# Kernel tuning notes

Measured on AMD Instinct MI355X. Metric: run time of the kernel, lower is better.

Reference implementation:

```python
import jax, jax.numpy as jnp
import numpy as np

N, E = 50000, 600000
IN, PE, H, L, K = 112, 16, 128, 64, 4


def setup_inputs() -> dict:
    key = jax.random.key(0)
    ks = jax.random.split(key, 8)
    x = jax.random.normal(ks[0], (N, IN), jnp.float32)
    edge_index = jax.random.randint(ks[1], (2, E), 0, N, dtype=jnp.int64)
    lap_pe = jax.random.normal(ks[2], (N, PE), jnp.float32)
    edge_weight = jax.random.uniform(ks[3], (E,), jnp.float32)
    s = lambda k, shp, fan: jax.random.normal(k, shp, jnp.float32) / np.sqrt(fan).astype(np.float32)
    W1 = s(ks[4], (K, IN + PE, H), IN + PE)
    b1 = jnp.zeros((H,), jnp.float32)
    W2 = s(ks[5], (K, H, H), H)
    b2 = jnp.zeros((H,), jnp.float32)
    Wmu = s(ks[6], (H, L), H)
    bmu = jnp.zeros((L,), jnp.float32)
    Wlv = s(ks[7], (H, L), H)
    blv = jnp.zeros((L,), jnp.float32)
    return dict(x=x, edge_index=edge_index, lap_pe=lap_pe, edge_weight=edge_weight,
                W1=W1, b1=b1, W2=W2, b2=b2, Wmu=Wmu, bmu=bmu, Wlv=Wlv, blv=blv)


def _cheb_conv(h, src, dst, w, W, b):
    """PyG ChebConv with precomputed scaled-Laplacian edge weights w.
    T_0 = h ; T_1 = That h ; T_k = 2 That T_{k-1} - T_{k-2}; out = sum_k T_k W_k + b."""
    n = h.shape[0]
    prop = lambda t: jax.ops.segment_sum(w[:, None] * t[src], dst, num_segments=n)
    Tx0 = h
    out = Tx0 @ W[0]
    Tx1 = prop(Tx0)
    out = out + Tx1 @ W[1]
    for k in range(2, W.shape[0]):
        Tx2 = 2.0 * prop(Tx1) - Tx0
        out = out + Tx2 @ W[k]
        Tx0, Tx1 = Tx1, Tx2
    return out + b


def reference(x, edge_index, lap_pe, edge_weight, W1, b1, W2, b2, Wmu, bmu, Wlv, blv):
    n = x.shape[0]
    src, dst = edge_index[0], edge_index[1]
    # sym-normalized Laplacian, lambda_max=2 -> That = L_sym - I = -D^-1/2 A D^-1/2
    deg = jax.ops.segment_sum(edge_weight, src, num_segments=n)
    dis = jnp.where(deg > 0, jax.lax.rsqrt(jnp.maximum(deg, 1e-12)), 0.0)
    w = -dis[src] * edge_weight * dis[dst]
    h = jnp.concatenate([x, lap_pe], axis=1)  # [N, in+pe]
    h = jax.nn.relu(_cheb_conv(h, src, dst, w, W1, b1))
    h = jax.nn.relu(_cheb_conv(h, src, dst, w, W2, b2))
    mu = h @ Wmu + bmu
    logvar = h @ Wlv + blv
    return (mu, logvar)
```

## Files before the change

kernel.cpp:

```cpp
#include <hip/hip_runtime.h>


typedef __bf16 bf16x8 __attribute__((ext_vector_type(8)));
typedef float f32x4 __attribute__((ext_vector_type(4)));
typedef unsigned int uint32;
typedef unsigned short ushort16;

__device__ inline ushort16 f2bf(float f) {
    uint32 x = __float_as_uint(f);
    uint32 r = x + 0x7fffu + ((x >> 16) & 1u);
    return (ushort16)(r >> 16);
}
__device__ inline float bflo(uint32 v) { return __uint_as_float(v << 16); }
__device__ inline float bfhi(uint32 v) { return __uint_as_float(v & 0xffff0000u); }


__global__ void k_deg_cnt(const int* __restrict__ src, const int* __restrict__ dst,
                          const float* __restrict__ ew, float* __restrict__ deg,
                          int* __restrict__ cnt, int* __restrict__ pos, int E) {
    int e = blockIdx.x * blockDim.x + threadIdx.x;
    if (e >= E) return;
    atomicAdd(&deg[src[e]], ew[e]);
    pos[e] = atomicAdd(&cnt[dst[e]], 1);
}

__global__ void k_scan_blk(const int* __restrict__ cnt, int* __restrict__ row_ptr,
                           int* __restrict__ blk_sums, int N) {
    __shared__ int wsum[4];
    const int tid = threadIdx.x;
    const int base = blockIdx.x * 1024 + tid * 4;
    int4 v = make_int4(0, 0, 0, 0);
    if (base + 3 < N) v = *(const int4*)&cnt[base];
    else {
        if (base + 0 < N) v.x = cnt[base + 0];
        if (base + 1 < N) v.y = cnt[base + 1];
        if (base + 2 < N) v.z = cnt[base + 2];
    }
    const int tsum = v.x + v.y + v.z + v.w;
    const int lane = tid & 63;
    const int wv = tid >> 6;
    int incl = tsum;
    #pragma unroll
    for (int off = 1; off < 64; off <<= 1) {
        int t = __shfl_up(incl, off);
        if (lane >= off) incl += t;
    }
    if (lane == 63) wsum[wv] = incl;
    __syncthreads();
    int woff = 0;
    #pragma unroll
    for (int w = 0; w < 4; ++w) if (w < wv) woff += wsum[w];
    const int excl = woff + incl - tsum;
    if (base + 0 < N) row_ptr[base + 0] = excl;
    if (base + 1 < N) row_ptr[base + 1] = excl + v.x;
    if (base + 2 < N) row_ptr[base + 2] = excl + v.x + v.y;
    if (base + 3 < N) row_ptr[base + 3] = excl + v.x + v.y + v.z;
    if (tid == 255) blk_sums[blockIdx.x] = woff + incl;
}

__global__ void k_scan_top(int* __restrict__ blk_sums, int* __restrict__ row_ptr,
                           int nblk, int N) {
    const int lane = threadIdx.x;
    int v = (lane < nblk) ? blk_sums[lane] : 0;
    int incl = v;
    #pragma unroll
    for (int off = 1; off < 64; off <<= 1) {
        int t = __shfl_up(incl, off);
        if (lane >= off) incl += t;
    }
    if (lane < nblk) blk_sums[lane] = incl - v;
    if (lane == 63) row_ptr[N] = incl;
}

__global__ void k_fix_dis(int* __restrict__ row_ptr, const int* __restrict__ blk_sums,
                          const float* __restrict__ deg, float* __restrict__ dis, int N) {
    int i = blockIdx.x * blockDim.x + threadIdx.x;
    if (i >= N) return;
    row_ptr[i] += blk_sums[i >> 10];
    float d = deg[i];
    dis[i] = d > 0.f ? rsqrtf(fmaxf(d, 1e-12f)) : 0.f;
}

__global__ void k_scatter(const int* __restrict__ src, const int* __restrict__ dst,
                          const float* __restrict__ ew, const float* __restrict__ dis,
                          const int* __restrict__ row_ptr, const int* __restrict__ pos,
                          int2* __restrict__ csr, int E) {
    int e = blockIdx.x * blockDim.x + threadIdx.x;
    if (e >= E) return;
    int s = src[e], d = dst[e];
    float wv = -dis[s] * ew[e] * dis[d];
    csr[row_ptr[d] + pos[e]] = make_int2(s, __float_as_int(wv));
}


__global__ void k_concat_bf16(const float* __restrict__ x, const float* __restrict__ pe,
                              uint32* __restrict__ h, int N) {
    int i4 = (blockIdx.x * blockDim.x + threadIdx.x) * 4;
    if (i4 >= N * 64) return;
    int node = i4 >> 6, p = i4 & 63;
    float4 fa, fb;
    if (p < 56) {
        const float* xp = &x[(size_t)node * 112 + p * 2];
        fa = *(const float4*)xp; fb = *(const float4*)(xp + 4);
    } else {
        const float* pp = &pe[(size_t)node * 16 + (p - 56) * 2];
        fa = *(const float4*)pp; fb = *(const float4*)(pp + 4);
    }
    int4 o;
    o.x = (uint32)f2bf(fa.x) | ((uint32)f2bf(fa.y) << 16);
    o.y = (uint32)f2bf(fa.z) | ((uint32)f2bf(fa.w) << 16);
    o.z = (uint32)f2bf(fb.x) | ((uint32)f2bf(fb.y) << 16);
    o.w = (uint32)f2bf(fb.z) | ((uint32)f2bf(fb.w) << 16);
    *(int4*)&h[i4] = o;
}


__device__ inline float wtrans(const float* __restrict__ W, int kb, size_t o) {
    switch (kb) {
        case 0:  return W[o] - W[o + 32768];
        case 1:  return W[o + 16384] - 3.f * W[o + 49152];
        case 2:  return 2.f * W[o + 32768];
        default: return 4.f * W[o + 49152];
    }
}

__global__ void k_pack_all(const float* __restrict__ W1, const float* __restrict__ W2,
                           const float* __restrict__ Wm, const float* __restrict__ Wl,
                           ushort16* __restrict__ W1p, ushort16* __restrict__ W2p,
                           ushort16* __restrict__ WHp) {
    int t = blockIdx.x * blockDim.x + threadIdx.x;
    uint32 v[8];
    if (t < 16384) {
        const float* W = (t < 8192) ? W1 : W2;
        ushort16* Wp = (t < 8192) ? W1p : W2p;
        int tt = t & 8191;
        int l = tt & 63, c = (tt >> 6) & 7, ks = tt >> 9;
        int kb = ks >> 2;
        int r0 = (ks & 3) * 32 + (l >> 4) * 8;
        int col = c * 16 + (l & 15);
        #pragma unroll
        for (int j = 0; j < 8; ++j)
            v[j] = f2bf(wtrans(W, kb, (size_t)(r0 + j) * 128 + col));
        uint4 o;
        o.x = v[0] | (v[1] << 16); o.y = v[2] | (v[3] << 16);
        o.z = v[4] | (v[5] << 16); o.w = v[6] | (v[7] << 16);
        *(uint4*)(Wp + (size_t)tt * 8) = o;
    } else if (t < 16384 + 2048) {
        int tt = t - 16384;
        int l = tt & 63, c = (tt >> 6) & 7, ks = tt >> 9;
        int k0 = ks * 32 + (l >> 4) * 8;
        int cc = c * 16 + (l & 15);
        const float* Ws = (cc < 64) ? Wm : Wl;
        int col = cc & 63;
        #pragma unroll
        for (int j = 0; j < 8; ++j) v[j] = f2bf(Ws[(size_t)(k0 + j) * 64 + col]);
        uint4 o;
        o.x = v[0] | (v[1] << 16); o.y = v[2] | (v[3] << 16);
        o.z = v[4] | (v[5] << 16); o.w = v[6] | (v[7] << 16);
        *(uint4*)(WHp + (size_t)tt * 8) = o;
    }
}


__global__ void k_prop(const uint32* __restrict__ tin, const int2* __restrict__ csr,
                       const int* __restrict__ row_ptr, uint32* __restrict__ out, int N) {
    int wid = (blockIdx.x * blockDim.x + threadIdx.x) >> 6;
    int lane = threadIdx.x & 63;
    if (wid >= N) return;
    int beg = row_ptr[wid], end = row_ptr[wid + 1];
    const int half = lane >> 5;
    const int fl = lane & 31;
    float a0 = 0.f, a1 = 0.f, a2 = 0.f, a3 = 0.f;
    for (int base = beg; base < end; base += 64) {
        int m = end - base; if (m > 64) m = 64;
        int2 ev = (lane < m) ? csr[base + lane] : make_int2(0, 0);
        for (int j = 0; j < m; j += 8) {
            #pragma unroll
            for (int u = 0; u < 4; ++u) {
                int idx = j + u * 2 + half;
                int s = __shfl(ev.x, idx);
                float w = __uint_as_float(__shfl(ev.y, idx));
                uint2 v = *(const uint2*)&tin[(size_t)s * 64 + fl * 2];
                a0 = fmaf(w, bflo(v.x), a0); a1 = fmaf(w, bfhi(v.x), a1);
                a2 = fmaf(w, bflo(v.y), a2); a3 = fmaf(w, bfhi(v.y), a3);
            }
        }
    }
    a0 += __shfl_xor(a0, 32);
    a1 += __shfl_xor(a1, 32);
    a2 += __shfl_xor(a2, 32);
    a3 += __shfl_xor(a3, 32);
    if (lane < 32) {
        uint2 o;
        o.x = (uint32)f2bf(a0) | ((uint32)f2bf(a1) << 16);
        o.y = (uint32)f2bf(a2) | ((uint32)f2bf(a3) << 16);
        *(uint2*)&out[(size_t)wid * 64 + fl * 2] = o;
    }
}


template<bool RELU>
__launch_bounds__(256)
__global__ void k_mfma_gemm512(const ushort16* __restrict__ t0, const ushort16* __restrict__ t1,
                               const ushort16* __restrict__ t2, const ushort16* __restrict__ t3,
                               const ushort16* __restrict__ Wp, const float* __restrict__ bias,
                               ushort16* __restrict__ C, int N) {
    const int lane = threadIdx.x & 63;
    const int wave = threadIdx.x >> 6;
    const int brow = blockIdx.x * 128 + wave * 32;
    int r0 = brow + (lane & 15);
    int r1 = r0 + 16;
    if (r0 >= N) r0 = N - 1;
    if (r1 >= N) r1 = N - 1;
    const int kg8 = (lane >> 4) * 8;
    f32x4 acc[2][8] = {};
    #pragma unroll
    for (int t = 0; t < 4; ++t) {
        const ushort16* __restrict__ A = (t == 0) ? t0 : (t == 1) ? t1 : (t == 2) ? t2 : t3;
        const ushort16* a0p = A + (size_t)r0 * 128 + kg8;
        const ushort16* a1p = A + (size_t)r1 * 128 + kg8;
        #pragma unroll
        for (int ks2 = 0; ks2 < 4; ++ks2) {
            bf16x8 a0 = *(const bf16x8*)(a0p + ks2 * 32);
            bf16x8 a1 = *(const bf16x8*)(a1p + ks2 * 32);
            const ushort16* bp = Wp + (size_t)((t * 4 + ks2) * 8 * 64 + lane) * 8;
            #pragma unroll
            for (int c = 0; c < 8; ++c) {
                bf16x8 b = *(const bf16x8*)(bp + c * 512);
                acc[0][c] = __builtin_amdgcn_mfma_f32_16x16x32_bf16(a0, b, acc[0][c], 0, 0, 0);
                acc[1][c] = __builtin_amdgcn_mfma_f32_16x16x32_bf16(a1, b, acc[1][c], 0, 0, 0);
            }
        }
    }
    const int col0 = lane & 15;
    const int rj = (lane >> 4) * 4;
    #pragma unroll
    for (int m = 0; m < 2; ++m) {
        #pragma unroll
        for (int c = 0; c < 8; ++c) {
            float bv = bias[c * 16 + col0];
            #pragma unroll
            for (int j = 0; j < 4; ++j) {
                int row = brow + m * 16 + rj + j;
                if (row < N) {
                    float v = acc[m][c][j] + bv;
                    if (RELU) v = fmaxf(v, 0.f);
                    C[(size_t)row * 128 + c * 16 + col0] = f2bf(v);
                }
            }
        }
    }
}


__launch_bounds__(256)
__global__ void k_mfma_head(const ushort16* __restrict__ A, const ushort16* __restrict__ Wp,
                            const float* __restrict__ bm, const float* __restrict__ bl,
                            float* __restrict__ out, int N) {
    const int lane = threadIdx.x & 63;
    const int wave = threadIdx.x >> 6;
    const int brow = blockIdx.x * 128 + wave * 32;
    int r0 = brow + (lane & 15);
    int r1 = r0 + 16;
    if (r0 >= N) r0 = N - 1;
    if (r1 >= N) r1 = N - 1;
    const int kg8 = (lane >> 4) * 8;
    f32x4 acc[2][8] = {};
    const ushort16* a0p = A + (size_t)r0 * 128 + kg8;
    const ushort16* a1p = A + (size_t)r1 * 128 + kg8;
    #pragma unroll
    for (int ks = 0; ks < 4; ++ks) {
        bf16x8 a0 = *(const bf16x8*)(a0p + ks * 32);
        bf16x8 a1 = *(const bf16x8*)(a1p + ks * 32);
        const ushort16* bp = Wp + (size_t)(ks * 8 * 64 + lane) * 8;
        #pragma unroll
        for (int c = 0; c < 8; ++c) {
            bf16x8 b = *(const bf16x8*)(bp + c * 512);
            acc[0][c] = __builtin_amdgcn_mfma_f32_16x16x32_bf16(a0, b, acc[0][c], 0, 0, 0);
            acc[1][c] = __builtin_amdgcn_mfma_f32_16x16x32_bf16(a1, b, acc[1][c], 0, 0, 0);
        }
    }
    const int col0 = lane & 15;
    const int rj = (lane >> 4) * 4;
    #pragma unroll
    for (int m = 0; m < 2; ++m) {
        #pragma unroll
        for (int c = 0; c < 8; ++c) {
            int gcol = (c & 3) * 16 + col0;
            float bv = (c < 4) ? bm[gcol] : bl[gcol];
            size_t hoff = (c < 4) ? 0 : (size_t)N * 64;
            #pragma unroll
            for (int j = 0; j < 4; ++j) {
                int row = brow + m * 16 + rj + j;
                if (row < N)
                    out[hoff + (size_t)row * 64 + gcol] = acc[m][c][j] + bv;
            }
        }
    }
}


extern "C" void kernel_launch(void* const* d_in, const int* in_sizes, int n_in,
                              void* d_out, int out_size, void* d_ws, size_t ws_size,
                              hipStream_t stream) {
    const float* x   = (const float*)d_in[0];
    const int*   ei  = (const int*)d_in[1];
    const float* pe  = (const float*)d_in[2];
    const float* ew  = (const float*)d_in[3];
    const float* W1  = (const float*)d_in[4];
    const float* b1  = (const float*)d_in[5];
    const float* W2  = (const float*)d_in[6];
    const float* b2  = (const float*)d_in[7];
    const float* Wmu = (const float*)d_in[8];
    const float* bmu = (const float*)d_in[9];
    const float* Wlv = (const float*)d_in[10];
    const float* blv = (const float*)d_in[11];

    const int N = in_sizes[0] / 112;
    const int E = in_sizes[1] / 2;
    const int* src = ei;
    const int* dst = ei + E;

    char* ws = (char*)d_ws;
    size_t off = 0;
    auto alloc = [&](size_t bytes) -> char* {
        char* p = ws + off;
        off = (off + bytes + 255) & ~(size_t)255;
        return p;
    };
    float* deg     = (float*)alloc((size_t)N * 4);
    int*   cnt     = (int*)  alloc((size_t)N * 4);
    float* dis     = (float*)alloc((size_t)N * 4);
    int*   row_ptr = (int*)  alloc((size_t)(N + 1) * 4);
    int*   blk_sums= (int*)  alloc((size_t)256 * 4);
    int*   pos     = (int*)  alloc((size_t)E * 4);
    int2*  csr     = (int2*) alloc((size_t)E * 8);
    ushort16* W1p  = (ushort16*)alloc((size_t)512 * 128 * 2);
    ushort16* W2p  = (ushort16*)alloc((size_t)512 * 128 * 2);
    ushort16* WHp  = (ushort16*)alloc((size_t)128 * 128 * 2);
    ushort16* B0 = (ushort16*)alloc((size_t)N * 128 * 2);
    ushort16* B1 = (ushort16*)alloc((size_t)N * 128 * 2);
    ushort16* B2 = (ushort16*)alloc((size_t)N * 128 * 2);
    ushort16* B3 = (ushort16*)alloc((size_t)N * 128 * 2);
    ushort16* B4 = (ushort16*)alloc((size_t)N * 128 * 2);

    hipMemsetAsync(deg, 0, (size_t)N * 4, stream);
    hipMemsetAsync(cnt, 0, (size_t)N * 4, stream);

    const int eb = (E + 255) / 256;
    const int nb = (N + 255) / 256;
    const int pb = (N + 3) / 4;
    const int gb = (N + 127) / 128;
    const int nblk = (N + 1023) / 1024;
    const int cb = (N * 64 + 1023) / 1024;

    k_deg_cnt<<<eb, 256, 0, stream>>>(src, dst, ew, deg, cnt, pos, E);
    k_scan_blk<<<nblk, 256, 0, stream>>>(cnt, row_ptr, blk_sums, N);
    k_scan_top<<<1, 64, 0, stream>>>(blk_sums, row_ptr, nblk, N);
    k_fix_dis<<<nb, 256, 0, stream>>>(row_ptr, blk_sums, deg, dis, N);
    k_scatter<<<eb, 256, 0, stream>>>(src, dst, ew, dis, row_ptr, pos, csr, E);
    k_concat_bf16<<<cb, 256, 0, stream>>>(x, pe, (uint32*)B0, N);
    k_pack_all<<<(16384 + 2048 + 255) / 256, 256, 0, stream>>>(W1, W2, Wmu, Wlv, W1p, W2p, WHp);

    k_prop<<<pb, 256, 0, stream>>>((uint32*)B0, csr, row_ptr, (uint32*)B1, N);
    k_prop<<<pb, 256, 0, stream>>>((uint32*)B1, csr, row_ptr, (uint32*)B2, N);
    k_prop<<<pb, 256, 0, stream>>>((uint32*)B2, csr, row_ptr, (uint32*)B3, N);
    k_mfma_gemm512<true><<<gb, 256, 0, stream>>>(B0, B1, B2, B3, W1p, b1, B4, N);

    k_prop<<<pb, 256, 0, stream>>>((uint32*)B4, csr, row_ptr, (uint32*)B0, N);
    k_prop<<<pb, 256, 0, stream>>>((uint32*)B0, csr, row_ptr, (uint32*)B1, N);
    k_prop<<<pb, 256, 0, stream>>>((uint32*)B1, csr, row_ptr, (uint32*)B2, N);
    k_mfma_gemm512<true><<<gb, 256, 0, stream>>>(B4, B0, B1, B2, W2p, b2, B3, N);

    k_mfma_head<<<gb, 256, 0, stream>>>(B3, WHp, bmu, blv, (float*)d_out, N);
}
```

Before: 313.2 us.

## Process two nodes per wave in propagation and split degree kernel into chunks

The propagation kernel now assigns one node to each 32-lane half-wave instead of one node per full wave. This removes the cross-half shuffle reduction and halves the number of waves launched. Separately, the degree/count kernel is launched as four sequential chunks over the edge range, which may change atomic contention patterns or serve as a timing probe. The per-node split exposes imbalance between the two halves of a wave when degrees differ.

```diff
diff --git a/kernel.cpp b/kernel.cpp
--- a/kernel.cpp
+++ b/kernel.cpp
@@ -17,9 +17,10 @@
 
 __global__ void k_deg_cnt(const int* __restrict__ src, const int* __restrict__ dst,
                           const float* __restrict__ ew, float* __restrict__ deg,
-                          int* __restrict__ cnt, int* __restrict__ pos, int E) {
-    int e = blockIdx.x * blockDim.x + threadIdx.x;
-    if (e >= E) return;
+                          int* __restrict__ cnt, int* __restrict__ pos,
+                          int e0, int e1) {
+    int e = e0 + blockIdx.x * blockDim.x + threadIdx.x;
+    if (e >= e1) return;
     atomicAdd(&deg[src[e]], ew[e]);
     pos[e] = atomicAdd(&cnt[dst[e]], 1);
 }
@@ -164,37 +165,35 @@
 
 __global__ void k_prop(const uint32* __restrict__ tin, const int2* __restrict__ csr,
                        const int* __restrict__ row_ptr, uint32* __restrict__ out, int N) {
-    int wid = (blockIdx.x * blockDim.x + threadIdx.x) >> 6;
+    int wave = (blockIdx.x * blockDim.x + threadIdx.x) >> 6;
     int lane = threadIdx.x & 63;
-    if (wid >= N) return;
-    int beg = row_ptr[wid], end = row_ptr[wid + 1];
     const int half = lane >> 5;
     const int fl = lane & 31;
+    int node = wave * 2 + half;
+    bool valid = node < N;
+    if (!valid) node = N - 1;
+    int beg = row_ptr[node];
+    int m = valid ? (row_ptr[node + 1] - beg) : 0;
     float a0 = 0.f, a1 = 0.f, a2 = 0.f, a3 = 0.f;
-    for (int base = beg; base < end; base += 64) {
-        int m = end - base; if (m > 64) m = 64;
-        int2 ev = (lane < m) ? csr[base + lane] : make_int2(0, 0);
-        for (int j = 0; j < m; j += 8) {
+    for (int base = 0; base < m; base += 32) {
+        int rem = m - base; if (rem > 32) rem = 32;
+        int2 ev = (fl < rem) ? csr[beg + base + fl] : make_int2(0, 0);
+        for (int j = 0; j < rem; j += 8) {
             #pragma unroll
-            for (int u = 0; u < 4; ++u) {
-                int idx = j + u * 2 + half;
-                int s = __shfl(ev.x, idx);
-                float w = __uint_as_float(__shfl(ev.y, idx));
+            for (int u = 0; u < 8; ++u) {
+                int s = __shfl(ev.x, half * 32 + j + u);
+                float w = __uint_as_float(__shfl(ev.y, half * 32 + j + u));
                 uint2 v = *(const uint2*)&tin[(size_t)s * 64 + fl * 2];
                 a0 = fmaf(w, bflo(v.x), a0); a1 = fmaf(w, bfhi(v.x), a1);
                 a2 = fmaf(w, bflo(v.y), a2); a3 = fmaf(w, bfhi(v.y), a3);
             }
         }
     }
-    a0 += __shfl_xor(a0, 32);
-    a1 += __shfl_xor(a1, 32);
-    a2 += __shfl_xor(a2, 32);
-    a3 += __shfl_xor(a3, 32);
-    if (lane < 32) {
+    if (valid) {
         uint2 o;
         o.x = (uint32)f2bf(a0) | ((uint32)f2bf(a1) << 16);
         o.y = (uint32)f2bf(a2) | ((uint32)f2bf(a3) << 16);
-        *(uint2*)&out[(size_t)wid * 64 + fl * 2] = o;
+        *(uint2*)&out[(size_t)node * 64 + fl * 2] = o;
     }
 }
 
@@ -347,18 +346,22 @@
     hipMemsetAsync(deg, 0, (size_t)N * 4, stream);
     hipMemsetAsync(cnt, 0, (size_t)N * 4, stream);
 
-    const int eb = (E + 255) / 256;
+    const int eb4 = (E / 4 + 255) / 256;
     const int nb = (N + 255) / 256;
-    const int pb = (N + 3) / 4;
+    const int pb = ((N + 1) / 2 + 3) / 4;
     const int gb = (N + 127) / 128;
     const int nblk = (N + 1023) / 1024;
     const int cb = (N * 64 + 1023) / 1024;
 
-    k_deg_cnt<<<eb, 256, 0, stream>>>(src, dst, ew, deg, cnt, pos, E);
+    for (int q = 0; q < 4; ++q) {
+        int e0 = (int)((size_t)E * q / 4);
+        int e1 = (int)((size_t)E * (q + 1) / 4);
+        k_deg_cnt<<<eb4, 256, 0, stream>>>(src, dst, ew, deg, cnt, pos, e0, e1);
+    }
     k_scan_blk<<<nblk, 256, 0, stream>>>(cnt, row_ptr, blk_sums, N);
     k_scan_top<<<1, 64, 0, stream>>>(blk_sums, row_ptr, nblk, N);
     k_fix_dis<<<nb, 256, 0, stream>>>(row_ptr, blk_sums, deg, dis, N);
-    k_scatter<<<eb, 256, 0, stream>>>(src, dst, ew, dis, row_ptr, pos, csr, E);
+    k_scatter<<<(E + 255) / 256, 256, 0, stream>>>(src, dst, ew, dis, row_ptr, pos, csr, E);
     k_concat_bf16<<<cb, 256, 0, stream>>>(x, pe, (uint32*)B0, N);
     k_pack_all<<<(16384 + 2048 + 255) / 256, 256, 0, stream>>>(W1, W2, Wmu, Wlv, W1p, W2p, WHp);
 
```

Result: no change. 312.0 us (-0.4%).
